# Optimization experiments

Measured on AMD Instinct MI355X. Metric: run time of the kernel, lower is better.

## Reference

```python
import jax, jax.numpy as jnp
import numpy as np

IN_CHANNELS = 64
N_NODES = 100000
N_POOLED = 50000
N_EDGES = 1250000


def setup_inputs() -> dict:
    key = jax.random.key(0)
    k1, k2, k3 = jax.random.split(key, 3)
    x_abstract = jax.random.normal(k1, (N_POOLED, IN_CHANNELS), dtype=jnp.float32)
    # pooling indices: unique subset of [0, N)
    perm = jax.random.permutation(k2, N_NODES)[:N_POOLED].astype(jnp.int32)
    edge_index = jax.random.randint(k3, (2, N_EDGES), 0, N_NODES, dtype=jnp.int32)
    return {
        "x_abstract": x_abstract,
        "perm": perm,
        "edge_index": edge_index,
        "original_num_nodes": N_NODES,
    }


def reference(x_abstract, perm, edge_index, original_num_nodes):
    N = original_num_nodes
    C = x_abstract.shape[1]
    # scatter pooled features back to original node slots
    x0 = jnp.zeros((N, C), dtype=x_abstract.dtype).at[perm].set(x_abstract)
    is_missing = jnp.ones((N,), dtype=bool).at[perm].set(False)

    # undirected view: every edge contributes both directions
    tgt = jnp.concatenate([edge_index[0], edge_index[1]])  # [2E]
    src = jnp.concatenate([edge_index[1], edge_index[0]])  # [2E]

    # deduplicate (tgt, src) pairs (torch.unique on neighbor ids) via lexsort + adjacent-diff mask
    order = jnp.lexsort((src, tgt))
    t_s = tgt[order]
    s_s = src[order]
    uniq = jnp.concatenate(
        [jnp.array([True]), (t_s[1:] != t_s[:-1]) | (s_s[1:] != s_s[:-1])]
    )
    # drop self loops (neighbor_ids != idx), weight 1 for each unique neighbor pair
    w = (uniq & (t_s != s_s)).astype(x_abstract.dtype)  # [2E]

    # scatter-mean of unique-neighbor features per target node
    feat_sum = jax.ops.segment_sum(x0[s_s] * w[:, None], t_s, num_segments=N)  # [N, C]
    cnt = jax.ops.segment_sum(w, t_s, num_segments=N)  # [N]
    mean = feat_sum / jnp.maximum(cnt, 1.0)[:, None]

    # only missing nodes with at least one neighbor get filled; others keep their value
    fill = is_missing & (cnt > 0)
    return jnp.where(fill[:, None], mean, x0)
```

## Files before the change

### kernel.cpp

```cpp
#include <hip/hip_runtime.h>
#include <stdint.h>

#define K_SLOTS 64

__global__ void scatter_kernel(const float* __restrict__ xab,
                               const int* __restrict__ perm,
                               float* __restrict__ out,
                               int* __restrict__ inv,
                               int Np, int C4) {
    int gid = blockIdx.x * blockDim.x + threadIdx.x;
    int j = gid / C4;
    int q = gid - j * C4;
    if (j >= Np) return;
    int p = perm[j];
    if (q == 0) inv[p] = j;
    const float4* src = (const float4*)xab + (size_t)j * C4;
    float4* dst = (float4*)out + (size_t)p * C4;
    dst[q] = src[q];
}

__global__ void fill_kernel(const int* __restrict__ ei, long long E,
                            const int* __restrict__ inv,
                            int* __restrict__ deg,
                            int* __restrict__ slot) {
    long long e = (long long)blockIdx.x * blockDim.x + threadIdx.x;
    if (e >= E) return;
    int a = ei[e];
    int b = ei[e + E];
    if (a == b) return;
    if (inv[a] < 0) {
        int pos = atomicAdd(&deg[a], 1);
        if (pos < K_SLOTS) slot[((size_t)a << 6) + pos] = b;
    }
    if (inv[b] < 0) {
        int pos = atomicAdd(&deg[b], 1);
        if (pos < K_SLOTS) slot[((size_t)b << 6) + pos] = a;
    }
}

__global__ void mean_kernel(const int* __restrict__ slot,
                            const int* __restrict__ deg,
                            const int* __restrict__ inv,
                            const float* __restrict__ xab,
                            float* __restrict__ out,
                            int N, int C) {
    int wid = (int)((blockIdx.x * (long long)blockDim.x + threadIdx.x) >> 6);
    int lane = threadIdx.x & 63;
    if (wid >= N) return;
    if (inv[wid] >= 0) return;
    int d = deg[wid];
    if (d > K_SLOTS) d = K_SLOTS;
    if (d <= 0) {
        for (int c = lane; c < C; c += 64) out[(size_t)wid * C + c] = 0.0f;
        return;
    }
    int s = -1, j = -1;
    if (lane < d) {
        s = slot[((size_t)wid << 6) + lane];
        j = inv[s];
    }
    bool dup = false;
    for (int k = 0; k < d - 1; ++k) {
        int v = __shfl(s, k, 64);
        if (lane > k && s == v) dup = true;
    }
    bool uniq = (lane < d) && !dup;
    unsigned long long um = __ballot(uniq);
    int cnt = __popcll(um);
    unsigned long long pm = __ballot(uniq && j >= 0);
    float rcnt = 1.0f / (float)cnt;
    for (int c0 = 0; c0 < C; c0 += 64) {
        int c = c0 + lane;
        float acc = 0.0f;
        unsigned long long m = pm;
        while (m) {
            int u = (int)__ffsll((unsigned long long)m) - 1;
            m &= m - 1;
            int jj = __shfl(j, u, 64);
            if (c < C) acc += xab[(size_t)jj * C + c];
        }
        if (c < C) out[(size_t)wid * C + c] = acc * rcnt;
    }
}

extern "C" void kernel_launch(void* const* d_in, const int* in_sizes, int n_in,
                              void* d_out, int out_size, void* d_ws, size_t ws_size,
                              hipStream_t stream) {
    const float* xab  = (const float*)d_in[0];
    const int*   perm = (const int*)d_in[1];
    const int*   ei   = (const int*)d_in[2];
    float* out = (float*)d_out;

    int Np = in_sizes[1];
    int C  = in_sizes[0] / Np;
    long long E = in_sizes[2] / 2;
    int N  = out_size / C;
    int C4 = C / 4;

    char* ws = (char*)d_ws;
    size_t off = 0;
    int* slot = (int*)(ws + off); off += (size_t)N * K_SLOTS * 4;
    int* deg  = (int*)(ws + off); off += (size_t)N * 4;
    int* inv  = (int*)(ws + off); off += (size_t)N * 4;

    hipMemsetAsync(deg, 0, (size_t)N * 4, stream);
    hipMemsetAsync(inv, 0xFF, (size_t)N * 4, stream);

    {
        long long threads = (long long)Np * C4;
        int blocks = (int)((threads + 255) / 256);
        scatter_kernel<<<blocks, 256, 0, stream>>>(xab, perm, out, inv, Np, C4);
    }
    {
        int blocks = (int)((E + 255) / 256);
        fill_kernel<<<blocks, 256, 0, stream>>>(ei, E, inv, deg, slot);
    }
    {
        long long threads = (long long)N * 64;
        int blocks = (int)((threads + 255) / 256);
        mean_kernel<<<blocks, 256, 0, stream>>>(slot, deg, inv, xab, out, N, C);
    }
}
```

Baseline: 223.2 us.

## Compact missing nodes into a worklist and batch gather loads in mean kernel

Adds a kernel that compacts the indices of missing nodes into a worklist using a wave ballot and one atomic per wave. The mean kernel then launches one wave per missing node instead of one per original node, which avoids waves that exit early on pooled nodes. It also unrolls the neighbour gather loop by four so several independent loads can be in flight at once. The cost is an extra kernel launch, a small memset and the M assumption (N minus Np equals the missing count); worklist order is nondeterministic but the outputs are not.

```diff
diff --git a/kernel.cpp b/kernel.cpp
--- a/kernel.cpp
+++ b/kernel.cpp
@@ -19,6 +19,22 @@
     dst[q] = src[q];
 }
 
+__global__ void mklist_kernel(const int* __restrict__ inv,
+                              int* __restrict__ work,
+                              unsigned* __restrict__ wn, int N) {
+    int i = blockIdx.x * blockDim.x + threadIdx.x;
+    int lane = threadIdx.x & 63;
+    bool miss = (i < N) && (inv[i] < 0);
+    unsigned long long m = __ballot(miss);
+    unsigned base = 0;
+    if (lane == 0 && m) base = atomicAdd(wn, (unsigned)__popcll(m));
+    base = __shfl((int)base, 0, 64);
+    if (miss) {
+        unsigned long long mask_lt = (1ull << lane) - 1ull;
+        work[base + __popcll(m & mask_lt)] = i;
+    }
+}
+
 __global__ void fill_kernel(const int* __restrict__ ei, long long E,
                             const int* __restrict__ inv,
                             int* __restrict__ deg,
@@ -38,25 +54,26 @@
     }
 }
 
-__global__ void mean_kernel(const int* __restrict__ slot,
+__global__ void mean_kernel(const int* __restrict__ work,
+                            const int* __restrict__ slot,
                             const int* __restrict__ deg,
                             const int* __restrict__ inv,
                             const float* __restrict__ xab,
                             float* __restrict__ out,
-                            int N, int C) {
+                            int M, int C) {
     int wid = (int)((blockIdx.x * (long long)blockDim.x + threadIdx.x) >> 6);
     int lane = threadIdx.x & 63;
-    if (wid >= N) return;
-    if (inv[wid] >= 0) return;
-    int d = deg[wid];
+    if (wid >= M) return;
+    int node = __builtin_amdgcn_readfirstlane(work[wid]);
+    int d = deg[node];
     if (d > K_SLOTS) d = K_SLOTS;
     if (d <= 0) {
-        for (int c = lane; c < C; c += 64) out[(size_t)wid * C + c] = 0.0f;
+        for (int c = lane; c < C; c += 64) out[(size_t)node * C + c] = 0.0f;
         return;
     }
     int s = -1, j = -1;
     if (lane < d) {
-        s = slot[((size_t)wid << 6) + lane];
+        s = slot[((size_t)node << 6) + lane];
         j = inv[s];
     }
     bool dup = false;
@@ -65,21 +82,31 @@
         if (lane > k && s == v) dup = true;
     }
     bool uniq = (lane < d) && !dup;
-    unsigned long long um = __ballot(uniq);
-    int cnt = __popcll(um);
+    int cnt = __popcll(__ballot(uniq));
     unsigned long long pm = __ballot(uniq && j >= 0);
     float rcnt = 1.0f / (float)cnt;
     for (int c0 = 0; c0 < C; c0 += 64) {
         int c = c0 + lane;
+        bool cc = (c < C);
         float acc = 0.0f;
         unsigned long long m = pm;
         while (m) {
-            int u = (int)__ffsll((unsigned long long)m) - 1;
-            m &= m - 1;
-            int jj = __shfl(j, u, 64);
-            if (c < C) acc += xab[(size_t)jj * C + c];
+            int u0 = (int)__ffsll(m) - 1; m &= m - 1;
+            int u1 = 0, u2 = 0, u3 = 0;
+            bool h1 = (m != 0); if (h1) { u1 = (int)__ffsll(m) - 1; m &= m - 1; }
+            bool h2 = (m != 0); if (h2) { u2 = (int)__ffsll(m) - 1; m &= m - 1; }
+            bool h3 = (m != 0); if (h3) { u3 = (int)__ffsll(m) - 1; m &= m - 1; }
+            int j0 = __shfl(j, u0, 64);
+            int j1 = __shfl(j, u1, 64);
+            int j2 = __shfl(j, u2, 64);
+            int j3 = __shfl(j, u3, 64);
+            float v0 = cc        ? xab[(size_t)j0 * C + c] : 0.0f;
+            float v1 = (cc & h1) ? xab[(size_t)j1 * C + c] : 0.0f;
+            float v2 = (cc & h2) ? xab[(size_t)j2 * C + c] : 0.0f;
+            float v3 = (cc & h3) ? xab[(size_t)j3 * C + c] : 0.0f;
+            acc += v0 + v1 + v2 + v3;
         }
-        if (c < C) out[(size_t)wid * C + c] = acc * rcnt;
+        if (cc) out[(size_t)node * C + c] = acc * rcnt;
     }
 }
 
@@ -96,15 +123,19 @@
     long long E = in_sizes[2] / 2;
     int N  = out_size / C;
     int C4 = C / 4;
+    int M  = N - Np;
 
     char* ws = (char*)d_ws;
     size_t off = 0;
     int* slot = (int*)(ws + off); off += (size_t)N * K_SLOTS * 4;
     int* deg  = (int*)(ws + off); off += (size_t)N * 4;
     int* inv  = (int*)(ws + off); off += (size_t)N * 4;
+    int* work = (int*)(ws + off); off += (size_t)M * 4;
+    unsigned* wn = (unsigned*)(ws + off); off += 256;
 
     hipMemsetAsync(deg, 0, (size_t)N * 4, stream);
     hipMemsetAsync(inv, 0xFF, (size_t)N * 4, stream);
+    hipMemsetAsync(wn, 0, 4, stream);
 
     {
         long long threads = (long long)Np * C4;
@@ -112,12 +143,16 @@
         scatter_kernel<<<blocks, 256, 0, stream>>>(xab, perm, out, inv, Np, C4);
     }
     {
+        int blocks = (N + 255) / 256;
+        mklist_kernel<<<blocks, 256, 0, stream>>>(inv, work, wn, N);
+    }
+    {
         int blocks = (int)((E + 255) / 256);
         fill_kernel<<<blocks, 256, 0, stream>>>(ei, E, inv, deg, slot);
     }
     {
-        long long threads = (long long)N * 64;
+        long long threads = (long long)M * 64;
         int blocks = (int)((threads + 255) / 256);
-        mean_kernel<<<blocks, 256, 0, stream>>>(slot, deg, inv, xab, out, N, C);
+        mean_kernel<<<blocks, 256, 0, stream>>>(work, slot, deg, inv, xab, out, M, C);
     }
 }
```

Result: no change. 222.0 us (-0.5%).
